# Optimization experiments

Hardware: AMD Instinct MI355X
Metric: run time of the kernel (lower is better)

## Reference

```python
import jax, jax.numpy as jnp
import numpy as np


def setup_inputs() -> dict:
    key = jax.random.key(0)
    k1, k2, k3 = jax.random.split(key, 3)
    B, U, D0, D1 = 256, 512, 512, 1024
    x = jax.random.normal(k1, (B, D0), dtype=jnp.float32)
    y = jax.random.normal(k2, (B, D1), dtype=jnp.float32)
    # Glorot-uniform-ish scale for the bilinear weight
    limit = np.sqrt(6.0 / (D0 + D1)).astype(np.float32)
    w = jax.random.uniform(k3, (U, D0, D1), dtype=jnp.float32, minval=-limit, maxval=limit)
    b = jnp.zeros((U,), dtype=jnp.float32)
    return {"x": x, "y": y, "w": w, "b": b}


def reference(x, y, w, b):
    # out[b,u] = sum_{i,j} x[b,i] * w[u,i,j] * y[b,j] + b[u]
    # Two chained GEMMs instead of materializing (B,U,D0,D1):
    xw = jnp.einsum('bi,uij->buj', x, w)   # (B, U, D1)
    out = jnp.einsum('buj,bj->bu', xw, y) + b  # (B, U)
    return out
```

## Files before the change

kernel.cpp:

```cpp
#include <hip/hip_runtime.h>
#include <hip/hip_bf16.h>

typedef float f32x4 __attribute__((ext_vector_type(4)));
typedef short s16x8 __attribute__((ext_vector_type(8)));

#define NB   256
#define NU   512
#define ND0  512
#define ND1  1024
#define WROW (ND0 * ND1)

#define WS_BYTES ((size_t)512 * 16 * 512 * 16)

__device__ __forceinline__ unsigned int f2bf_pk(float a, float b) {
  __hip_bfloat16 ha = __float2bfloat16(a);
  __hip_bfloat16 hb = __float2bfloat16(b);
  unsigned short ua, ub;
  __builtin_memcpy(&ua, &ha, 2);
  __builtin_memcpy(&ub, &hb, 2);
  return (unsigned int)ua | ((unsigned int)ub << 16);
}

__device__ __forceinline__ void block_sync_lds() {
  asm volatile("s_waitcnt lgkmcnt(0)" ::: "memory");
  __builtin_amdgcn_s_barrier();
}

__global__ __launch_bounds__(256) void init_out(const float* __restrict__ bias,
                                                float* __restrict__ out) {
  int idx = blockIdx.x * 256 + threadIdx.x;
  out[idx] = bias[idx & (NU - 1)];
}

__global__ __launch_bounds__(256) void reduce_ws(
    const float* __restrict__ bias, const f32x4* __restrict__ ws4,
    float* __restrict__ out) {
  const int g  = blockIdx.x * 256 + threadIdx.x;
  const int u  = g & 511;
  const int bh = g >> 9;
  const int wm = bh >> 5, mf = (bh >> 2) & 7, lk = bh & 3;
  const int ntile = u >> 7, wn = (u >> 5) & 3, nf = (u >> 4) & 1, l15 = u & 15;
  const int t  = (wm * 4 + wn) * 64 + lk * 16 + l15;
  const size_t base = (size_t)(mf * 2 + nf) * 512 + t;

  f32x4 s0 = {0, 0, 0, 0}, s1 = {0, 0, 0, 0};
#pragma unroll 8
  for (int ic = 0; ic < 128; ic += 2) {
    s0 += ws4[base + (size_t)((ic + 0) * 4 + ntile) * (16 * 512)];
    s1 += ws4[base + (size_t)((ic + 1) * 4 + ntile) * (16 * 512)];
  }
  f32x4 s = s0 + s1;
  const float bv = bias[u];
  const int b0 = bh * 4;
#pragma unroll
  for (int r = 0; r < 4; ++r)
    out[(size_t)(b0 + r) * NU + u] = s[r] + bv;
}

__global__ __launch_bounds__(512, 4) void bilinear_kern(
    const float* __restrict__ x, const float* __restrict__ y,
    const float* __restrict__ w, float* __restrict__ out,
    float* __restrict__ ws, int use_ws) {
  __shared__ char Alds[32768];
  __shared__ char Wlds[16384];

  const int t    = threadIdx.x;
  const int lane = t & 63;
  const int l15  = lane & 15;
  const int lk   = lane >> 4;
  const int wid  = t >> 6;
  const int wm   = wid >> 2;
  const int wn   = wid & 3;

  const int nt    = blockIdx.x & 3;
  const int ic    = blockIdx.x >> 2;
  const int off   = (nt << 4) | (ic & 15);
  const int ucol0 = nt * 128 + wn * 32;

  f32x4 acc[8][2];
#pragma unroll
  for (int mf = 0; mf < 8; ++mf)
#pragma unroll
    for (int nf = 0; nf < 2; ++nf)
#pragma unroll
      for (int r = 0; r < 4; ++r) acc[mf][nf][r] = 0.0f;

  const int ar   = t >> 4;
  const int aswz = (ar & 7) << 4;
  const int awr  = ar * 128 + ((l15 * 8) ^ aswz);
  const float* yb = y + (size_t)ar * ND1 + l15 * 4;

  const int wrb = wid * 16 + lk;
  const float* wq = w + (size_t)(nt * 128 + wrb) * WROW + l15 * 4;

  const int afswz = (l15 & 7) << 4;

  f32x4 wv[4], wvn[4];
  const int ii0 = ic * 4 + (off >> 4);
  {
    const float* p0 = wq + (size_t)ii0 * ND1 + (off & 15) * 64;
#pragma unroll
    for (int q = 0; q < 4; ++q)
      wv[q] = __builtin_nontemporal_load((const f32x4*)(p0 + (size_t)q * 4 * WROW));
  }
  float xv[8];
#pragma unroll
  for (int p = 0; p < 8; ++p)
    xv[p] = x[(size_t)(ar + 32 * p) * ND0 + ii0];

  for (int it = 0; it < 64; ++it) {
    const int s  = (it + off) & 63;
    const int j0 = (s & 15) * 64;

    block_sync_lds();

#pragma unroll
    for (int g = 0; g < 2; ++g) {
      f32x4 v[4];
#pragma unroll
      for (int pp = 0; pp < 4; ++pp)
        v[pp] = *(const f32x4*)(yb + (size_t)(g * 4 + pp) * 32 * ND1 + j0);
#pragma unroll
      for (int pp = 0; pp < 4; ++pp) {
        const int p = g * 4 + pp;
        unsigned long long pk =
            (unsigned long long)f2bf_pk(xv[p] * v[pp][0], xv[p] * v[pp][1]) |
            ((unsigned long long)f2bf_pk(xv[p] * v[pp][2], xv[p] * v[pp][3]) << 32);
        *(unsigned long long*)(Alds + awr + p * 4096) = pk;
      }
    }

#pragma unroll
    for (int q = 0; q < 4; ++q) {
      const int row  = wrb + 4 * q;
      const int byte = row * 128 + ((l15 * 8) ^ ((row & 7) << 4));
      unsigned long long pk =
          (unsigned long long)f2bf_pk(wv[q][0], wv[q][1]) |
          ((unsigned long long)f2bf_pk(wv[q][2], wv[q][3]) << 32);
      *(unsigned long long*)(Wlds + byte) = pk;
    }

    if (it < 63) {
      const int sn = (s + 1) & 63;
      const int ii = ic * 4 + (sn >> 4);
      const int jn = (sn & 15) * 64;
      const float* pn = wq + (size_t)ii * ND1 + jn;
#pragma unroll
      for (int q = 0; q < 4; ++q)
        wvn[q] = __builtin_nontemporal_load((const f32x4*)(pn + (size_t)q * 4 * WROW));
      if ((s & 15) == 15) {
#pragma unroll
        for (int pp = 0; pp < 8; ++pp)
          xv[pp] = x[(size_t)(ar + 32 * pp) * ND0 + ii];
      }
    }

    block_sync_lds();

#pragma unroll
    for (int ks = 0; ks < 2; ++ks) {
      const int kcol = ks * 64;
      s16x8 bf[2];
#pragma unroll
      for (int nf = 0; nf < 2; ++nf) {
        const int row = wn * 32 + nf * 16 + l15;
        bf[nf] = *(const s16x8*)(Wlds + row * 128 + ((kcol + lk * 16) ^ afswz));
      }
#pragma unroll
      for (int mf = 0; mf < 8; ++mf) {
        const int row = wm * 128 + mf * 16 + l15;
        s16x8 af = *(const s16x8*)(Alds + row * 128 + ((kcol + lk * 16) ^ afswz));
        acc[mf][0] = __builtin_amdgcn_mfma_f32_16x16x32_bf16(af, bf[0], acc[mf][0], 0, 0, 0);
        acc[mf][1] = __builtin_amdgcn_mfma_f32_16x16x32_bf16(af, bf[1], acc[mf][1], 0, 0, 0);
      }
    }

#pragma unroll
    for (int q = 0; q < 4; ++q) wv[q] = wvn[q];
  }

  if (use_ws) {
    f32x4* ws4 = (f32x4*)ws + (size_t)blockIdx.x * (16 * 512) + t;
#pragma unroll
    for (int mf = 0; mf < 8; ++mf)
#pragma unroll
      for (int nf = 0; nf < 2; ++nf)
        __builtin_nontemporal_store(acc[mf][nf], ws4 + (mf * 2 + nf) * 512);
  } else {
#pragma unroll
    for (int mf = 0; mf < 8; ++mf) {
      const int grow = wm * 128 + mf * 16 + lk * 4;
#pragma unroll
      for (int nf = 0; nf < 2; ++nf) {
        const int gcol = ucol0 + nf * 16 + l15;
#pragma unroll
        for (int r = 0; r < 4; ++r) {
          atomicAdd(out + (size_t)(grow + r) * NU + gcol, acc[mf][nf][r]);
        }
      }
    }
  }
}

extern "C" void kernel_launch(void* const* d_in, const int* in_sizes, int n_in,
                              void* d_out, int out_size, void* d_ws, size_t ws_size,
                              hipStream_t stream) {
  const float* x    = (const float*)d_in[0];
  const float* y    = (const float*)d_in[1];
  const float* w    = (const float*)d_in[2];
  const float* bias = (const float*)d_in[3];
  float* out = (float*)d_out;

  const bool use_ws = (d_ws != nullptr) && (ws_size >= WS_BYTES);
  if (use_ws) {
    bilinear_kern<<<512, 512, 0, stream>>>(x, y, w, out, (float*)d_ws, 1);
    reduce_ws<<<128, 256, 0, stream>>>(bias, (const f32x4*)d_ws, out);
  } else {
    init_out<<<512, 256, 0, stream>>>(bias, out);
    bilinear_kern<<<512, 512, 0, stream>>>(x, y, w, out, nullptr, 0);
  }
}
```

Baseline: 292.3 us.

## Stream W tiles directly into LDS with triple-buffered async global_load_lds

Weight tiles now go straight from global memory into a three-slot LDS ring via global_load_lds, two stages ahead of use. They stay fp32 in LDS and are converted to bf16 when read as MFMA operands, rather than being held in registers and converted before storing. The loop is split into half-K steps (128 iterations of 32 columns), with waits tied to vmcnt so loads overlap compute, and the per-block staggered start offset is dropped. This raises LDS use to 80KB per block, which cuts occupancy. It also adds per-read conversion work and removes the staggering that spread DRAM access across blocks.

```diff
diff --git a/kernel.cpp b/kernel.cpp
--- a/kernel.cpp
+++ b/kernel.cpp
@@ -24,6 +24,12 @@
 __device__ __forceinline__ void block_sync_lds() {
   asm volatile("s_waitcnt lgkmcnt(0)" ::: "memory");
   __builtin_amdgcn_s_barrier();
+}
+
+__device__ __forceinline__ void glds16(const void* g, void* l) {
+  __builtin_amdgcn_global_load_lds(
+      (const __attribute__((address_space(1))) void*)g,
+      (__attribute__((address_space(3))) void*)l, 16, 0, 0);
 }
 
 __global__ __launch_bounds__(256) void init_out(const float* __restrict__ bias,
@@ -61,8 +67,8 @@
     const float* __restrict__ x, const float* __restrict__ y,
     const float* __restrict__ w, float* __restrict__ out,
     float* __restrict__ ws, int use_ws) {
-  __shared__ char Alds[32768];
-  __shared__ char Wlds[16384];
+  __shared__ __align__(16) char Alds[32768];
+  __shared__ __align__(16) char Wlds[49152];
 
   const int t    = threadIdx.x;
   const int lane = t & 63;
@@ -74,7 +80,6 @@
 
   const int nt    = blockIdx.x & 3;
   const int ic    = blockIdx.x >> 2;
-  const int off   = (nt << 4) | (ic & 15);
   const int ucol0 = nt * 128 + wn * 32;
 
   f32x4 acc[8][2];
@@ -86,97 +91,110 @@
       for (int r = 0; r < 4; ++r) acc[mf][nf][r] = 0.0f;
 
   const int ar   = t >> 4;
-  const int aswz = (ar & 7) << 4;
-  const int awr  = ar * 128 + ((l15 * 8) ^ aswz);
+  const int awr  = ar * 128 + ((l15 * 8) ^ ((ar & 7) << 4));
   const float* yb = y + (size_t)ar * ND1 + l15 * 4;
 
-  const int wrb = wid * 16 + lk;
-  const float* wq = w + (size_t)(nt * 128 + wrb) * WROW + l15 * 4;
+  const int rl = lane >> 3;
+  const int cs = ((lane & 7) ^ rl) * 4;
+  const float* wg0 = w + (size_t)(nt * 128 + wid * 16 + rl) * WROW + cs;
+  const float* wg1 = w + (size_t)(nt * 128 + wid * 16 + 8 + rl) * WROW + cs;
+  char* const wdst = Wlds + wid * 2048;
 
   const int afswz = (l15 & 7) << 4;
 
-  f32x4 wv[4], wvn[4];
-  const int ii0 = ic * 4 + (off >> 4);
+  float xv[8];
+#pragma unroll
+  for (int p = 0; p < 8; ++p)
+    xv[p] = x[(size_t)(ar + 32 * p) * ND0 + ic * 4];
   {
-    const float* p0 = wq + (size_t)ii0 * ND1 + (off & 15) * 64;
-#pragma unroll
-    for (int q = 0; q < 4; ++q)
-      wv[q] = __builtin_nontemporal_load((const f32x4*)(p0 + (size_t)q * 4 * WROW));
-  }
-  float xv[8];
-#pragma unroll
-  for (int p = 0; p < 8; ++p)
-    xv[p] = x[(size_t)(ar + 32 * p) * ND0 + ii0];
-
-  for (int it = 0; it < 64; ++it) {
-    const int s  = (it + off) & 63;
-    const int j0 = (s & 15) * 64;
-
+    const size_t o0 = (size_t)(ic * 4) * ND1;
+    glds16(wg0 + o0, wdst);
+    glds16(wg1 + o0, wdst + 1024);
+    const size_t o1 = o0 + 32;
+    glds16(wg0 + o1, wdst + 16384);
+    glds16(wg1 + o1, wdst + 16384 + 1024);
+  }
+
+  int cur = 0;
+  for (int it = 0; it < 128; ++it) {
     block_sync_lds();
 
-#pragma unroll
-    for (int g = 0; g < 2; ++g) {
-      f32x4 v[4];
-#pragma unroll
-      for (int pp = 0; pp < 4; ++pp)
-        v[pp] = *(const f32x4*)(yb + (size_t)(g * 4 + pp) * 32 * ND1 + j0);
-#pragma unroll
-      for (int pp = 0; pp < 4; ++pp) {
-        const int p = g * 4 + pp;
-        unsigned long long pk =
-            (unsigned long long)f2bf_pk(xv[p] * v[pp][0], xv[p] * v[pp][1]) |
-            ((unsigned long long)f2bf_pk(xv[p] * v[pp][2], xv[p] * v[pp][3]) << 32);
-        *(unsigned long long*)(Alds + awr + p * 4096) = pk;
+    if ((it & 31) == 0 && it) {
+      const int ii = ic * 4 + (it >> 5);
+#pragma unroll
+      for (int p = 0; p < 8; ++p)
+        xv[p] = x[(size_t)(ar + 32 * p) * ND0 + ii];
+    }
+
+    const int nb = (cur >= 1) ? (cur - 1) : 2;
+    char* dst = Wlds + nb * 16384 + wid * 2048;
+
+    if ((it & 1) == 0) {
+      const int j0 = ((it >> 1) & 15) * 64;
+#pragma unroll
+      for (int g = 0; g < 2; ++g) {
+        f32x4 v[4];
+#pragma unroll
+        for (int pp = 0; pp < 4; ++pp)
+          v[pp] = *(const f32x4*)(yb + (size_t)(g * 4 + pp) * 32 * ND1 + j0);
+        if (g == 0 && it < 126) {
+          const int tn = it + 2;
+          const size_t on = (size_t)(ic * 4 + (tn >> 5)) * ND1
+                          + (size_t)((tn & 31) * 32);
+          glds16(wg0 + on, dst);
+          glds16(wg1 + on, dst + 1024);
+        }
+#pragma unroll
+        for (int pp = 0; pp < 4; ++pp) {
+          const int p = g * 4 + pp;
+          unsigned long long pk =
+              (unsigned long long)f2bf_pk(xv[p] * v[pp][0], xv[p] * v[pp][1]) |
+              ((unsigned long long)f2bf_pk(xv[p] * v[pp][2], xv[p] * v[pp][3]) << 32);
+          *(unsigned long long*)(Alds + awr + p * 4096) = pk;
+        }
       }
-    }
-
-#pragma unroll
-    for (int q = 0; q < 4; ++q) {
-      const int row  = wrb + 4 * q;
-      const int byte = row * 128 + ((l15 * 8) ^ ((row & 7) << 4));
-      unsigned long long pk =
-          (unsigned long long)f2bf_pk(wv[q][0], wv[q][1]) |
-          ((unsigned long long)f2bf_pk(wv[q][2], wv[q][3]) << 32);
-      *(unsigned long long*)(Wlds + byte) = pk;
-    }
-
-    if (it < 63) {
-      const int sn = (s + 1) & 63;
-      const int ii = ic * 4 + (sn >> 4);
-      const int jn = (sn & 15) * 64;
-      const float* pn = wq + (size_t)ii * ND1 + jn;
-#pragma unroll
-      for (int q = 0; q < 4; ++q)
-        wvn[q] = __builtin_nontemporal_load((const f32x4*)(pn + (size_t)q * 4 * WROW));
-      if ((s & 15) == 15) {
-#pragma unroll
-        for (int pp = 0; pp < 8; ++pp)
-          xv[pp] = x[(size_t)(ar + 32 * pp) * ND0 + ii];
+    } else {
+      if (it < 126) {
+        const int tn = it + 2;
+        const size_t on = (size_t)(ic * 4 + (tn >> 5)) * ND1
+                        + (size_t)((tn & 31) * 32);
+        glds16(wg0 + on, dst);
+        glds16(wg1 + on, dst + 1024);
       }
     }
 
-    block_sync_lds();
-
-#pragma unroll
-    for (int ks = 0; ks < 2; ++ks) {
-      const int kcol = ks * 64;
-      s16x8 bf[2];
-#pragma unroll
-      for (int nf = 0; nf < 2; ++nf) {
-        const int row = wn * 32 + nf * 16 + l15;
-        bf[nf] = *(const s16x8*)(Wlds + row * 128 + ((kcol + lk * 16) ^ afswz));
-      }
-#pragma unroll
-      for (int mf = 0; mf < 8; ++mf) {
-        const int row = wm * 128 + mf * 16 + l15;
-        s16x8 af = *(const s16x8*)(Alds + row * 128 + ((kcol + lk * 16) ^ afswz));
-        acc[mf][0] = __builtin_amdgcn_mfma_f32_16x16x32_bf16(af, bf[0], acc[mf][0], 0, 0, 0);
-        acc[mf][1] = __builtin_amdgcn_mfma_f32_16x16x32_bf16(af, bf[1], acc[mf][1], 0, 0, 0);
-      }
-    }
-
-#pragma unroll
-    for (int q = 0; q < 4; ++q) wv[q] = wvn[q];
+    if (it < 126)
+      asm volatile("s_waitcnt vmcnt(4) lgkmcnt(0)" ::: "memory");
+    else if (it == 126)
+      asm volatile("s_waitcnt vmcnt(2) lgkmcnt(0)" ::: "memory");
+    else
+      asm volatile("s_waitcnt vmcnt(0) lgkmcnt(0)" ::: "memory");
+    __builtin_amdgcn_s_barrier();
+
+    const char* Wcur = Wlds + cur * 16384;
+    const int kc = (it & 1) * 64;
+    s16x8 bfr[2];
+#pragma unroll
+    for (int nf = 0; nf < 2; ++nf) {
+      const int row = wn * 32 + nf * 16 + l15;
+      const int r7  = row & 7;
+      const char* base = Wcur + row * 128;
+      const int c0 = lk * 2;
+      f32x4 wlo = *(const f32x4*)(base + ((c0 ^ r7) << 4));
+      f32x4 whi = *(const f32x4*)(base + (((c0 + 1) ^ r7) << 4));
+      unsigned int pk[4] = { f2bf_pk(wlo[0], wlo[1]), f2bf_pk(wlo[2], wlo[3]),
+                             f2bf_pk(whi[0], whi[1]), f2bf_pk(whi[2], whi[3]) };
+      __builtin_memcpy(&bfr[nf], pk, 16);
+    }
+#pragma unroll
+    for (int mf = 0; mf < 8; ++mf) {
+      const int row = wm * 128 + mf * 16 + l15;
+      s16x8 af = *(const s16x8*)(Alds + row * 128 + ((kc + lk * 16) ^ afswz));
+      acc[mf][0] = __builtin_amdgcn_mfma_f32_16x16x32_bf16(af, bfr[0], acc[mf][0], 0, 0, 0);
+      acc[mf][1] = __builtin_amdgcn_mfma_f32_16x16x32_bf16(af, bfr[1], acc[mf][1], 0, 0, 0);
+    }
+
+    cur = (cur == 2) ? 0 : cur + 1;
   }
 
   if (use_ws) {
```

After: 420.7 us. 1.44x slower.
